# Performance work log

Hardware: AMD Instinct MI355X
Metric: run time of the kernel (lower is better)

The kernel has to match this reference:

```python
import jax, jax.numpy as jnp
import numpy as np

B, H, W, C = 4, 64, 64, 256
C8 = C // 8

def setup_inputs() -> dict:
    key = jax.random.key(0)
    k1, k2, k3, k4 = jax.random.split(key, 4)
    # glorot-uniform-ish init for 1x1 conv kernels stored as [Cin, Cout]
    def glorot(k, cin, cout):
        lim = np.sqrt(6.0 / (cin + cout)).astype(np.float32)
        return jax.random.uniform(k, (cin, cout), jnp.float32, -lim, lim)
    return {
        "x": jax.random.normal(k1, (B, H, W, C), jnp.float32),
        "kernel_f": glorot(k2, C, C8),
        "kernel_g": glorot(k3, C, C8),
        "kernel_h": glorot(k4, C, C),
        "gamma": jnp.zeros((1,), jnp.float32),
    }

def reference(x, kernel_f, kernel_g, kernel_h, gamma):
    b, h, w, c = x.shape
    n = h * w
    xf = x.reshape(b, n, c)                       # [B, N, C]
    # 1x1 convs == per-position matmuls
    f = jnp.einsum('bnc,cd->bnd', xf, kernel_f)   # [B, N, C/8]
    g = jnp.einsum('bnc,cd->bnd', xf, kernel_g)   # [B, N, C/8]
    hh = jnp.einsum('bnc,cd->bnd', xf, kernel_h)  # [B, N, C]
    s = jnp.einsum('bnd,bmd->bnm', g, f)          # [B, N, N]
    beta = jax.nn.softmax(s, axis=-1)
    o = jnp.einsum('bnm,bmc->bnc', beta, hh)      # [B, N, C]
    o = o.reshape(b, h, w, c)
    return gamma * o + x
```

## Files before the change

### kernel.cpp

```cpp
#include <hip/hip_runtime.h>
#include <hip/hip_bf16.h>

typedef __bf16 bf16x8 __attribute__((ext_vector_type(8)));
typedef float f32x4 __attribute__((ext_vector_type(4)));
typedef float f32x16 __attribute__((ext_vector_type(16)));
typedef unsigned short u16;
typedef unsigned int u32;

__device__ __forceinline__ u16 f2bf_rne(float f){
  union { float f; u32 u; } v; v.f = f;
  u32 r = v.u + 0x7fffu + ((v.u >> 16) & 1u);
  return (u16)(r >> 16);
}
__device__ __forceinline__ u32 pack2(float a, float b){
  return __builtin_amdgcn_perm(__float_as_uint(a), __float_as_uint(b), 0x03020706u);
}
#define BARRIER_LGKM() asm volatile("s_waitcnt lgkmcnt(0)\n\ts_barrier" ::: "memory")

__global__ __launch_bounds__(512) void prep_kernel(
    const float* __restrict__ Wf, const float* __restrict__ Wg,
    const float* __restrict__ Wh, u16* __restrict__ Wfrag){
  const int cc = blockIdx.x;
  const int t = threadIdx.x;
  const int kk = t >> 6, lane = t & 63;
  const int L = lane & 15, quad = lane >> 4;
  const int n = cc * 16 + L;
  u32 pk[4];
  #pragma unroll
  for (int j2 = 0; j2 < 4; ++j2){
    float v[2];
    #pragma unroll
    for (int h = 0; h < 2; ++h){
      int k = kk * 32 + quad * 8 + j2 * 2 + h;
      if (n < 256)      v[h] = Wh[k * 256 + n];
      else if (n < 288) v[h] = Wf[k * 32 + (n - 256)];
      else              v[h] = Wg[k * 32 + (n - 288)];
    }
    pk[j2] = (u32)f2bf_rne(v[0]) | ((u32)f2bf_rne(v[1]) << 16);
  }
  uint4* dst = (uint4*)(Wfrag + ((size_t)(cc * 8 + kk) * 64 + lane) * 8);
  *dst = make_uint4(pk[0], pk[1], pk[2], pk[3]);
}

__global__ __launch_bounds__(512) void proj_kernel(
    const float* __restrict__ x, const u16* __restrict__ Wfrag,
    u16* __restrict__ Qg, u16* __restrict__ Kg, u16* __restrict__ Vfrag)
{
  __shared__ __align__(16) u16 smem[256 * 72];
  u16 (*xb)[264] = (u16(*)[264])smem;
  u16 (*Vr)[72]  = (u16(*)[72])smem;

  const int tid = threadIdx.x;
  const int lane = tid & 63, wave = tid >> 6;
  const int L = lane & 15, quad = lane >> 4;
  const int rowgrp = wave >> 1, colhalf = wave & 1;
  const int n0 = blockIdx.x * 64;

  const float4* xsrc = (const float4*)(x + (size_t)n0 * 256);
  #pragma unroll
  for (int j = 0; j < 8; ++j){
    int idx = j * 512 + tid;
    int row = idx >> 6, col4 = idx & 63;
    float4 v = xsrc[idx];
    u32 p0 = (u32)f2bf_rne(v.x) | ((u32)f2bf_rne(v.y) << 16);
    u32 p1 = (u32)f2bf_rne(v.z) | ((u32)f2bf_rne(v.w) << 16);
    *(uint2*)&xb[row][col4 * 4] = make_uint2(p0, p1);
  }
  __syncthreads();

  f32x4 acc[10];
  #pragma unroll
  for (int cc = 0; cc < 10; ++cc) acc[cc] = (f32x4){0.f, 0.f, 0.f, 0.f};

  #pragma unroll
  for (int kk = 0; kk < 8; ++kk){
    bf16x8 a = *(const bf16x8*)&xb[rowgrp * 16 + L][kk * 32 + quad * 8];
    #pragma unroll
    for (int cc = 0; cc < 10; ++cc){
      int ccg = colhalf * 10 + cc;
      bf16x8 bfr = *(const bf16x8*)(Wfrag + ((size_t)(ccg * 8 + kk) * 64 + lane) * 8);
      acc[cc] = __builtin_amdgcn_mfma_f32_16x16x32_bf16(a, bfr, acc[cc], 0, 0, 0);
    }
  }

  if (colhalf){
    #pragma unroll
    for (int cc = 6; cc < 10; ++cc){
      int ccg = 10 + cc;
      u16* dst = (ccg < 18) ? Kg : Qg;
      float sc = (ccg < 18) ? 1.0f : 1.44269504088896f;
      int c = (ccg & 1) * 16 + L;
      #pragma unroll
      for (int r = 0; r < 4; ++r){
        int row = n0 + rowgrp * 16 + quad * 4 + r;
        dst[(size_t)row * 32 + c] = f2bf_rne(acc[cc][r] * sc);
      }
    }
  }

  __syncthreads();

  {
    const int cmax = colhalf ? 6 : 10;
    for (int cc = 0; cc < cmax; ++cc){
      int ccg = colhalf * 10 + cc;
      int c = ccg * 16 + L;
      #pragma unroll
      for (int r = 0; r < 4; ++r){
        int tn = rowgrp * 16 + quad * 4 + r;
        int p  = ((tn & 15) << 2) | (tn >> 4);
        Vr[c][p] = f2bf_rne(acc[cc][r]);
      }
    }
  }
  __syncthreads();

  u16* Vblk = Vfrag + (size_t)blockIdx.x * (256 * 64);
  #pragma unroll
  for (int i = 0; i < 4; ++i){
    int idx = i * 512 + tid;
    *(uint4*)(Vblk + (size_t)idx * 8) = *(const uint4*)&Vr[idx & 255][(idx >> 8) * 8];
  }
}

__global__ __launch_bounds__(512) void flash_kernel(
    const u16* __restrict__ Qg, const u16* __restrict__ Kg, const u16* __restrict__ Vfrag,
    const float* __restrict__ x, const float* __restrict__ gamma, float* __restrict__ out)
{
  constexpr float SH = -92.33248261689366f;
  __shared__ __align__(16) char smem[65536];
  u16 (*Plds)[2][64][72] = (u16 (*)[2][64][72])smem;
  float (*Osh)[256] = (float (*)[256])smem;
  __shared__ float Lsh[2][64];

  const int tid = threadIdx.x, lane = tid & 63, wave = tid >> 6;
  const int L = lane & 15, quad = lane >> 4;
  const int m32 = lane & 31, h32 = lane >> 5;
  const int half = wave >> 2, wv = wave & 3;

  const int id = blockIdx.x;
  const int xcd = id & 7;
  const int b = xcd >> 1;
  const int qt = (xcd & 1) * 32 + (id >> 3);
  const int q0 = qt * 64;

  const u16* Qb = Qg + (size_t)(b * 4096) * 32;
  const u16* Kb = Kg + (size_t)(b * 4096) * 32;
  const u16* Vb = Vfrag + (size_t)b * (64 * 256 * 64);
  const float gm = gamma[0];

  const int g0 = half * 32;

  bf16x8 qa = *(const bf16x8*)(Qb + (size_t)(q0 + wv * 16 + L) * 32 + quad * 8);
  const u16* kp0 = Kb + (size_t)(g0 * 64 + L) * 32 + quad * 8;
  bf16x8 kc0 = *(const bf16x8*)(kp0);
  bf16x8 kc1 = *(const bf16x8*)(kp0 + 512);
  bf16x8 kc2 = *(const bf16x8*)(kp0 + 1024);
  bf16x8 kc3 = *(const bf16x8*)(kp0 + 1536);

  bf16x8 vfc[8];
  {
    const u16* Vt = Vb + (size_t)g0 * (256 * 64);
    #pragma unroll
    for (int ks = 0; ks < 4; ++ks){
      const u16* vrow = Vt + (size_t)((ks * 2 + h32) * 256 + wv * 64 + m32) * 8;
      vfc[ks * 2]     = *(const bf16x8*)(vrow);
      vfc[ks * 2 + 1] = *(const bf16x8*)(vrow + 32 * 8);
    }
  }

  f32x16 acc[4];
  #pragma unroll
  for (int t = 0; t < 4; ++t)
    #pragma unroll
    for (int i = 0; i < 16; ++i) acc[t][i] = 0.f;
  float lsum[4] = {0.f, 0.f, 0.f, 0.f};
  const f32x4 zero = (f32x4){0.f, 0.f, 0.f, 0.f};

  for (int kt = 0; kt < 32; ++kt){
    const int g = g0 + kt;
    u16 (*Pw)[72] = Plds[half][kt & 1];

    f32x4 s0 = __builtin_amdgcn_mfma_f32_16x16x32_bf16(qa, kc0, zero, 0, 0, 0);
    f32x4 s1 = __builtin_amdgcn_mfma_f32_16x16x32_bf16(qa, kc1, zero, 0, 0, 0);
    f32x4 s2 = __builtin_amdgcn_mfma_f32_16x16x32_bf16(qa, kc2, zero, 0, 0, 0);
    f32x4 s3 = __builtin_amdgcn_mfma_f32_16x16x32_bf16(qa, kc3, zero, 0, 0, 0);

    if (kt < 31){
      const u16* kpn = Kb + (size_t)((g + 1) * 64 + L) * 32 + quad * 8;
      kc0 = *(const bf16x8*)(kpn);
      kc1 = *(const bf16x8*)(kpn + 512);
      kc2 = *(const bf16x8*)(kpn + 1024);
      kc3 = *(const bf16x8*)(kpn + 1536);
    }

    #pragma unroll
    for (int r = 0; r < 4; ++r){
      float p0 = __builtin_amdgcn_exp2f(s0[r] + SH);
      float p1 = __builtin_amdgcn_exp2f(s1[r] + SH);
      float p2 = __builtin_amdgcn_exp2f(s2[r] + SH);
      float p3 = __builtin_amdgcn_exp2f(s3[r] + SH);
      lsum[r] += (p0 + p1) + (p2 + p3);
      *(uint2*)&Pw[wv * 16 + quad * 4 + r][L * 4] =
          make_uint2(pack2(p0, p1), pack2(p2, p3));
    }

    BARRIER_LGKM();

    #pragma unroll
    for (int ks = 0; ks < 4; ++ks){
      bf16x8 af0 = *(const bf16x8*)&Pw[m32][ks * 16 + h32 * 8];
      bf16x8 af1 = *(const bf16x8*)&Pw[32 + m32][ks * 16 + h32 * 8];
      acc[0] = __builtin_amdgcn_mfma_f32_32x32x16_bf16(af0, vfc[ks*2],   acc[0], 0, 0, 0);
      acc[1] = __builtin_amdgcn_mfma_f32_32x32x16_bf16(af0, vfc[ks*2+1], acc[1], 0, 0, 0);
      acc[2] = __builtin_amdgcn_mfma_f32_32x32x16_bf16(af1, vfc[ks*2],   acc[2], 0, 0, 0);
      acc[3] = __builtin_amdgcn_mfma_f32_32x32x16_bf16(af1, vfc[ks*2+1], acc[3], 0, 0, 0);
    }

    if (kt < 31){
      const u16* Vn = Vb + (size_t)(g + 1) * (256 * 64);
      #pragma unroll
      for (int ks = 0; ks < 4; ++ks){
        const u16* vrow = Vn + (size_t)((ks * 2 + h32) * 256 + wv * 64 + m32) * 8;
        vfc[ks * 2]     = *(const bf16x8*)(vrow);
        vfc[ks * 2 + 1] = *(const bf16x8*)(vrow + 32 * 8);
      }
    }
  }

  BARRIER_LGKM();

  #pragma unroll
  for (int r = 0; r < 4; ++r){
    lsum[r] += __shfl_xor(lsum[r], 1);
    lsum[r] += __shfl_xor(lsum[r], 2);
    lsum[r] += __shfl_xor(lsum[r], 4);
    lsum[r] += __shfl_xor(lsum[r], 8);
  }
  if (L == 0){
    #pragma unroll
    for (int r = 0; r < 4; ++r) Lsh[half][wv * 16 + quad * 4 + r] = lsum[r];
  }
  if (half == 1){
    #pragma unroll
    for (int t = 0; t < 4; ++t){
      const int qi = t >> 1, ci = t & 1;
      #pragma unroll
      for (int rg = 0; rg < 16; ++rg){
        int row = qi * 32 + (rg & 3) + 8 * (rg >> 2) + 4 * h32;
        Osh[row][wv * 64 + ci * 32 + m32] = acc[t][rg];
      }
    }
  }
  __syncthreads();
  if (wave == 0){
    float li = gm / (Lsh[0][lane] + Lsh[1][lane]);
    Lsh[0][lane] = li;
  }
  __syncthreads();
  if (half == 0){
    #pragma unroll
    for (int t = 0; t < 4; ++t){
      const int qi = t >> 1, ci = t & 1;
      #pragma unroll
      for (int rg = 0; rg < 16; ++rg){
        int row = qi * 32 + (rg & 3) + 8 * (rg >> 2) + 4 * h32;
        int col = wv * 64 + ci * 32 + m32;
        Osh[row][col] = (acc[t][rg] + Osh[row][col]) * Lsh[0][row];
      }
    }
  }
  __syncthreads();
  const size_t base = ((size_t)(b * 4096) + q0) * 256;
  const float4* xs = (const float4*)(x + base);
  float4* od = (float4*)(out + base);
  const float4* Of = (const float4*)&Osh[0][0];
  #pragma unroll
  for (int i = 0; i < 8; ++i){
    int idx = i * 512 + tid;
    float4 o = Of[idx], xv = xs[idx];
    o.x += xv.x; o.y += xv.y; o.z += xv.z; o.w += xv.w;
    od[idx] = o;
  }
}

extern "C" void kernel_launch(void* const* d_in, const int* in_sizes, int n_in,
                              void* d_out, int out_size, void* d_ws, size_t ws_size,
                              hipStream_t stream) {
  const float* x     = (const float*)d_in[0];
  const float* Wf    = (const float*)d_in[1];
  const float* Wg    = (const float*)d_in[2];
  const float* Wh    = (const float*)d_in[3];
  const float* gamma = (const float*)d_in[4];
  float* out = (float*)d_out;

  u16* p = (u16*)d_ws;
  u16* Qg    = p;  p += 16384 * 32;
  u16* Kg    = p;  p += 16384 * 32;
  u16* Vfrag = p;  p += 4 * 64 * 256 * 64;
  u16* Wfrag = p;  p += 20 * 8 * 64 * 8;

  prep_kernel<<<20, 512, 0, stream>>>(Wf, Wg, Wh, Wfrag);
  proj_kernel<<<256, 512, 0, stream>>>(x, Wfrag, Qg, Kg, Vfrag);
  flash_kernel<<<256, 512, 0, stream>>>(Qg, Kg, Vfrag, x, gamma, out);
}
```

Baseline: 151.3 us.

## Split flash attention KV range across four wave groups with 1024-thread blocks

New measurement: 233.0 us. 53.9% more time.

```diff
diff --git a/kernel.cpp b/kernel.cpp
--- a/kernel.cpp
+++ b/kernel.cpp
@@ -123,20 +123,20 @@
   }
 }
 
-__global__ __launch_bounds__(512) void flash_kernel(
+__global__ __launch_bounds__(1024) void flash_kernel(
     const u16* __restrict__ Qg, const u16* __restrict__ Kg, const u16* __restrict__ Vfrag,
     const float* __restrict__ x, const float* __restrict__ gamma, float* __restrict__ out)
 {
   constexpr float SH = -92.33248261689366f;
-  __shared__ __align__(16) char smem[65536];
+  __shared__ __align__(16) char smem[73728];
   u16 (*Plds)[2][64][72] = (u16 (*)[2][64][72])smem;
   float (*Osh)[256] = (float (*)[256])smem;
-  __shared__ float Lsh[2][64];
+  __shared__ float Lsh[4][64];
 
   const int tid = threadIdx.x, lane = tid & 63, wave = tid >> 6;
   const int L = lane & 15, quad = lane >> 4;
   const int m32 = lane & 31, h32 = lane >> 5;
-  const int half = wave >> 2, wv = wave & 3;
+  const int quarter = wave >> 2, wv = wave & 3;
 
   const int id = blockIdx.x;
   const int xcd = id & 7;
@@ -149,7 +149,7 @@
   const u16* Vb = Vfrag + (size_t)b * (64 * 256 * 64);
   const float gm = gamma[0];
 
-  const int g0 = half * 32;
+  const int g0 = quarter * 16;
 
   bf16x8 qa = *(const bf16x8*)(Qb + (size_t)(q0 + wv * 16 + L) * 32 + quad * 8);
   const u16* kp0 = Kb + (size_t)(g0 * 64 + L) * 32 + quad * 8;
@@ -177,16 +177,16 @@
   float lsum[4] = {0.f, 0.f, 0.f, 0.f};
   const f32x4 zero = (f32x4){0.f, 0.f, 0.f, 0.f};
 
-  for (int kt = 0; kt < 32; ++kt){
+  for (int kt = 0; kt < 16; ++kt){
     const int g = g0 + kt;
-    u16 (*Pw)[72] = Plds[half][kt & 1];
+    u16 (*Pw)[72] = Plds[quarter][kt & 1];
 
     f32x4 s0 = __builtin_amdgcn_mfma_f32_16x16x32_bf16(qa, kc0, zero, 0, 0, 0);
     f32x4 s1 = __builtin_amdgcn_mfma_f32_16x16x32_bf16(qa, kc1, zero, 0, 0, 0);
     f32x4 s2 = __builtin_amdgcn_mfma_f32_16x16x32_bf16(qa, kc2, zero, 0, 0, 0);
     f32x4 s3 = __builtin_amdgcn_mfma_f32_16x16x32_bf16(qa, kc3, zero, 0, 0, 0);
 
-    if (kt < 31){
+    if (kt < 15){
       const u16* kpn = Kb + (size_t)((g + 1) * 64 + L) * 32 + quad * 8;
       kc0 = *(const bf16x8*)(kpn);
       kc1 = *(const bf16x8*)(kpn + 512);
@@ -217,7 +217,7 @@
       acc[3] = __builtin_amdgcn_mfma_f32_32x32x16_bf16(af1, vfc[ks*2+1], acc[3], 0, 0, 0);
     }
 
-    if (kt < 31){
+    if (kt < 15){
       const u16* Vn = Vb + (size_t)(g + 1) * (256 * 64);
       #pragma unroll
       for (int ks = 0; ks < 4; ++ks){
@@ -227,8 +227,6 @@
       }
     }
   }
-
-  BARRIER_LGKM();
 
   #pragma unroll
   for (int r = 0; r < 4; ++r){
@@ -239,9 +237,12 @@
   }
   if (L == 0){
     #pragma unroll
-    for (int r = 0; r < 4; ++r) Lsh[half][wv * 16 + quad * 4 + r] = lsum[r];
-  }
-  if (half == 1){
+    for (int r = 0; r < 4; ++r) Lsh[quarter][wv * 16 + quad * 4 + r] = lsum[r];
+  }
+
+  BARRIER_LGKM();
+
+  if (quarter == 3){
     #pragma unroll
     for (int t = 0; t < 4; ++t){
       const int qi = t >> 1, ci = t & 1;
@@ -252,13 +253,36 @@
       }
     }
   }
-  __syncthreads();
-  if (wave == 0){
-    float li = gm / (Lsh[0][lane] + Lsh[1][lane]);
-    Lsh[0][lane] = li;
-  }
-  __syncthreads();
-  if (half == 0){
+  float li_w0 = 0.f;
+  if (wave == 0)
+    li_w0 = gm / (Lsh[0][lane] + Lsh[1][lane] + Lsh[2][lane] + Lsh[3][lane]);
+  __syncthreads();
+  if (wave == 0) Lsh[0][lane] = li_w0;
+  if (quarter == 2){
+    #pragma unroll
+    for (int t = 0; t < 4; ++t){
+      const int qi = t >> 1, ci = t & 1;
+      #pragma unroll
+      for (int rg = 0; rg < 16; ++rg){
+        int row = qi * 32 + (rg & 3) + 8 * (rg >> 2) + 4 * h32;
+        Osh[row][wv * 64 + ci * 32 + m32] += acc[t][rg];
+      }
+    }
+  }
+  __syncthreads();
+  if (quarter == 1){
+    #pragma unroll
+    for (int t = 0; t < 4; ++t){
+      const int qi = t >> 1, ci = t & 1;
+      #pragma unroll
+      for (int rg = 0; rg < 16; ++rg){
+        int row = qi * 32 + (rg & 3) + 8 * (rg >> 2) + 4 * h32;
+        Osh[row][wv * 64 + ci * 32 + m32] += acc[t][rg];
+      }
+    }
+  }
+  __syncthreads();
+  if (quarter == 0){
     #pragma unroll
     for (int t = 0; t < 4; ++t){
       const int qi = t >> 1, ci = t & 1;
@@ -276,8 +300,8 @@
   float4* od = (float4*)(out + base);
   const float4* Of = (const float4*)&Osh[0][0];
   #pragma unroll
-  for (int i = 0; i < 8; ++i){
-    int idx = i * 512 + tid;
+  for (int i = 0; i < 4; ++i){
+    int idx = i * 1024 + tid;
     float4 o = Of[idx], xv = xs[idx];
     o.x += xv.x; o.y += xv.y; o.z += xv.z; o.w += xv.w;
     od[idx] = o;
@@ -302,5 +326,5 @@
 
   prep_kernel<<<20, 512, 0, stream>>>(Wf, Wg, Wh, Wfrag);
   proj_kernel<<<256, 512, 0, stream>>>(x, Wfrag, Qg, Kg, Vfrag);
-  flash_kernel<<<256, 512, 0, stream>>>(Qg, Kg, Vfrag, x, gamma, out);
-}
+  flash_kernel<<<256, 1024, 0, stream>>>(Qg, Kg, Vfrag, x, gamma, out);
+}
```

## Split flash kernel over channel halves and stage V tiles through LDS

Applied to the files above, without the earlier changes.

After: 182.9 us. +20.9%, slower.

```diff
diff --git a/kernel.cpp b/kernel.cpp
--- a/kernel.cpp
+++ b/kernel.cpp
@@ -15,7 +15,10 @@
 __device__ __forceinline__ u32 pack2(float a, float b){
   return __builtin_amdgcn_perm(__float_as_uint(a), __float_as_uint(b), 0x03020706u);
 }
-#define BARRIER_LGKM() asm volatile("s_waitcnt lgkmcnt(0)\n\ts_barrier" ::: "memory")
+__device__ __forceinline__ void load_lds16(const void* g, void* l){
+  __builtin_amdgcn_global_load_lds((const __attribute__((address_space(1))) void*)g,
+                                   (__attribute__((address_space(3))) void*)l, 16, 0, 0);
+}
 
 __global__ __launch_bounds__(512) void prep_kernel(
     const float* __restrict__ Wf, const float* __restrict__ Wg,
@@ -128,71 +131,66 @@
     const float* __restrict__ x, const float* __restrict__ gamma, float* __restrict__ out)
 {
   constexpr float SH = -92.33248261689366f;
-  __shared__ __align__(16) char smem[65536];
-  u16 (*Plds)[2][64][72] = (u16 (*)[2][64][72])smem;
-  float (*Osh)[256] = (float (*)[256])smem;
+  __shared__ __align__(16) u16 Vlds[2][8192];
+  __shared__ __align__(16) u16 Plds[2][2][64][72];
   __shared__ float Lsh[2][64];
 
   const int tid = threadIdx.x, lane = tid & 63, wave = tid >> 6;
   const int L = lane & 15, quad = lane >> 4;
   const int m32 = lane & 31, h32 = lane >> 5;
-  const int half = wave >> 2, wv = wave & 3;
+  const int qg = wave >> 2, wv = wave & 3;
 
   const int id = blockIdx.x;
   const int xcd = id & 7;
   const int b = xcd >> 1;
-  const int qt = (xcd & 1) * 32 + (id >> 3);
-  const int q0 = qt * 64;
+  const int ch = (id >> 3) & 1;
+  const int qt = (xcd & 1) * 16 + (id >> 4);
+  const int q0 = qt * 128;
 
   const u16* Qb = Qg + (size_t)(b * 4096) * 32;
   const u16* Kb = Kg + (size_t)(b * 4096) * 32;
   const u16* Vb = Vfrag + (size_t)b * (64 * 256 * 64);
   const float gm = gamma[0];
 
-  const int g0 = half * 32;
-
-  bf16x8 qa = *(const bf16x8*)(Qb + (size_t)(q0 + wv * 16 + L) * 32 + quad * 8);
-  const u16* kp0 = Kb + (size_t)(g0 * 64 + L) * 32 + quad * 8;
+  bf16x8 qa = *(const bf16x8*)(Qb + (size_t)(q0 + qg * 64 + wv * 16 + L) * 32 + quad * 8);
+
+  {
+    const u16* src = Vb + wave * 2048 + ch * 1024 + lane * 8;
+    load_lds16(src,       &Vlds[0][wave * 1024]);
+    load_lds16(src + 512, &Vlds[0][wave * 1024 + 512]);
+    asm volatile("" ::: "memory");
+  }
+  const u16* kp0 = Kb + (size_t)(0 * 64 + L) * 32 + quad * 8;
   bf16x8 kc0 = *(const bf16x8*)(kp0);
   bf16x8 kc1 = *(const bf16x8*)(kp0 + 512);
   bf16x8 kc2 = *(const bf16x8*)(kp0 + 1024);
   bf16x8 kc3 = *(const bf16x8*)(kp0 + 1536);
 
-  bf16x8 vfc[8];
-  {
-    const u16* Vt = Vb + (size_t)g0 * (256 * 64);
-    #pragma unroll
-    for (int ks = 0; ks < 4; ++ks){
-      const u16* vrow = Vt + (size_t)((ks * 2 + h32) * 256 + wv * 64 + m32) * 8;
-      vfc[ks * 2]     = *(const bf16x8*)(vrow);
-      vfc[ks * 2 + 1] = *(const bf16x8*)(vrow + 32 * 8);
-    }
-  }
-
-  f32x16 acc[4];
-  #pragma unroll
-  for (int t = 0; t < 4; ++t)
+  f32x16 acc[2];
+  #pragma unroll
+  for (int t = 0; t < 2; ++t)
     #pragma unroll
     for (int i = 0; i < 16; ++i) acc[t][i] = 0.f;
   float lsum[4] = {0.f, 0.f, 0.f, 0.f};
   const f32x4 zero = (f32x4){0.f, 0.f, 0.f, 0.f};
 
-  for (int kt = 0; kt < 32; ++kt){
-    const int g = g0 + kt;
-    u16 (*Pw)[72] = Plds[half][kt & 1];
+  int buf = 0;
+  for (int kt = 0; kt < 63; ++kt){
+    u16 (*Pw)[72] = Plds[qg][kt & 1];
 
     f32x4 s0 = __builtin_amdgcn_mfma_f32_16x16x32_bf16(qa, kc0, zero, 0, 0, 0);
     f32x4 s1 = __builtin_amdgcn_mfma_f32_16x16x32_bf16(qa, kc1, zero, 0, 0, 0);
     f32x4 s2 = __builtin_amdgcn_mfma_f32_16x16x32_bf16(qa, kc2, zero, 0, 0, 0);
     f32x4 s3 = __builtin_amdgcn_mfma_f32_16x16x32_bf16(qa, kc3, zero, 0, 0, 0);
 
-    if (kt < 31){
-      const u16* kpn = Kb + (size_t)((g + 1) * 64 + L) * 32 + quad * 8;
+    {
+      const u16* kpn = Kb + (size_t)((kt + 1) * 64 + L) * 32 + quad * 8;
       kc0 = *(const bf16x8*)(kpn);
       kc1 = *(const bf16x8*)(kpn + 512);
       kc2 = *(const bf16x8*)(kpn + 1024);
       kc3 = *(const bf16x8*)(kpn + 1536);
     }
+    asm volatile("" ::: "memory");
 
     #pragma unroll
     for (int r = 0; r < 4; ++r){
@@ -205,30 +203,54 @@
           make_uint2(pack2(p0, p1), pack2(p2, p3));
     }
 
-    BARRIER_LGKM();
-
+    asm volatile("s_waitcnt vmcnt(4) lgkmcnt(0)\n\ts_barrier" ::: "memory");
+
+    {
+      const u16* Vn = Vb + (size_t)(kt + 1) * 16384 + wave * 2048 + ch * 1024 + lane * 8;
+      load_lds16(Vn,       &Vlds[buf ^ 1][wave * 1024]);
+      load_lds16(Vn + 512, &Vlds[buf ^ 1][wave * 1024 + 512]);
+      asm volatile("" ::: "memory");
+    }
+
+    const u16* Vls = &Vlds[buf][0];
     #pragma unroll
     for (int ks = 0; ks < 4; ++ks){
+      bf16x8 vf  = *(const bf16x8*)(Vls + ((ks * 2 + h32) * 128 + wv * 32 + m32) * 8);
       bf16x8 af0 = *(const bf16x8*)&Pw[m32][ks * 16 + h32 * 8];
       bf16x8 af1 = *(const bf16x8*)&Pw[32 + m32][ks * 16 + h32 * 8];
-      acc[0] = __builtin_amdgcn_mfma_f32_32x32x16_bf16(af0, vfc[ks*2],   acc[0], 0, 0, 0);
-      acc[1] = __builtin_amdgcn_mfma_f32_32x32x16_bf16(af0, vfc[ks*2+1], acc[1], 0, 0, 0);
-      acc[2] = __builtin_amdgcn_mfma_f32_32x32x16_bf16(af1, vfc[ks*2],   acc[2], 0, 0, 0);
-      acc[3] = __builtin_amdgcn_mfma_f32_32x32x16_bf16(af1, vfc[ks*2+1], acc[3], 0, 0, 0);
-    }
-
-    if (kt < 31){
-      const u16* Vn = Vb + (size_t)(g + 1) * (256 * 64);
-      #pragma unroll
-      for (int ks = 0; ks < 4; ++ks){
-        const u16* vrow = Vn + (size_t)((ks * 2 + h32) * 256 + wv * 64 + m32) * 8;
-        vfc[ks * 2]     = *(const bf16x8*)(vrow);
-        vfc[ks * 2 + 1] = *(const bf16x8*)(vrow + 32 * 8);
-      }
-    }
-  }
-
-  BARRIER_LGKM();
+      acc[0] = __builtin_amdgcn_mfma_f32_32x32x16_bf16(af0, vf, acc[0], 0, 0, 0);
+      acc[1] = __builtin_amdgcn_mfma_f32_32x32x16_bf16(af1, vf, acc[1], 0, 0, 0);
+    }
+    buf ^= 1;
+  }
+
+  {
+    u16 (*Pw)[72] = Plds[qg][63 & 1];
+    f32x4 s0 = __builtin_amdgcn_mfma_f32_16x16x32_bf16(qa, kc0, zero, 0, 0, 0);
+    f32x4 s1 = __builtin_amdgcn_mfma_f32_16x16x32_bf16(qa, kc1, zero, 0, 0, 0);
+    f32x4 s2 = __builtin_amdgcn_mfma_f32_16x16x32_bf16(qa, kc2, zero, 0, 0, 0);
+    f32x4 s3 = __builtin_amdgcn_mfma_f32_16x16x32_bf16(qa, kc3, zero, 0, 0, 0);
+    #pragma unroll
+    for (int r = 0; r < 4; ++r){
+      float p0 = __builtin_amdgcn_exp2f(s0[r] + SH);
+      float p1 = __builtin_amdgcn_exp2f(s1[r] + SH);
+      float p2 = __builtin_amdgcn_exp2f(s2[r] + SH);
+      float p3 = __builtin_amdgcn_exp2f(s3[r] + SH);
+      lsum[r] += (p0 + p1) + (p2 + p3);
+      *(uint2*)&Pw[wv * 16 + quad * 4 + r][L * 4] =
+          make_uint2(pack2(p0, p1), pack2(p2, p3));
+    }
+    asm volatile("s_waitcnt vmcnt(0) lgkmcnt(0)\n\ts_barrier" ::: "memory");
+    const u16* Vls = &Vlds[buf][0];
+    #pragma unroll
+    for (int ks = 0; ks < 4; ++ks){
+      bf16x8 vf  = *(const bf16x8*)(Vls + ((ks * 2 + h32) * 128 + wv * 32 + m32) * 8);
+      bf16x8 af0 = *(const bf16x8*)&Pw[m32][ks * 16 + h32 * 8];
+      bf16x8 af1 = *(const bf16x8*)&Pw[32 + m32][ks * 16 + h32 * 8];
+      acc[0] = __builtin_amdgcn_mfma_f32_32x32x16_bf16(af0, vf, acc[0], 0, 0, 0);
+      acc[1] = __builtin_amdgcn_mfma_f32_32x32x16_bf16(af1, vf, acc[1], 0, 0, 0);
+    }
+  }
 
   #pragma unroll
   for (int r = 0; r < 4; ++r){
@@ -239,48 +261,22 @@
   }
   if (L == 0){
     #pragma unroll
-    for (int r = 0; r < 4; ++r) Lsh[half][wv * 16 + quad * 4 + r] = lsum[r];
-  }
-  if (half == 1){
-    #pragma unroll
-    for (int t = 0; t < 4; ++t){
-      const int qi = t >> 1, ci = t & 1;
-      #pragma unroll
-      for (int rg = 0; rg < 16; ++rg){
-        int row = qi * 32 + (rg & 3) + 8 * (rg >> 2) + 4 * h32;
-        Osh[row][wv * 64 + ci * 32 + m32] = acc[t][rg];
-      }
-    }
+    for (int r = 0; r < 4; ++r) Lsh[qg][wv * 16 + quad * 4 + r] = lsum[r];
   }
   __syncthreads();
-  if (wave == 0){
-    float li = gm / (Lsh[0][lane] + Lsh[1][lane]);
-    Lsh[0][lane] = li;
-  }
-  __syncthreads();
-  if (half == 0){
-    #pragma unroll
-    for (int t = 0; t < 4; ++t){
-      const int qi = t >> 1, ci = t & 1;
-      #pragma unroll
-      for (int rg = 0; rg < 16; ++rg){
-        int row = qi * 32 + (rg & 3) + 8 * (rg >> 2) + 4 * h32;
-        int col = wv * 64 + ci * 32 + m32;
-        Osh[row][col] = (acc[t][rg] + Osh[row][col]) * Lsh[0][row];
-      }
-    }
-  }
-  __syncthreads();
-  const size_t base = ((size_t)(b * 4096) + q0) * 256;
-  const float4* xs = (const float4*)(x + base);
-  float4* od = (float4*)(out + base);
-  const float4* Of = (const float4*)&Osh[0][0];
-  #pragma unroll
-  for (int i = 0; i < 8; ++i){
-    int idx = i * 512 + tid;
-    float4 o = Of[idx], xv = xs[idx];
-    o.x += xv.x; o.y += xv.y; o.z += xv.z; o.w += xv.w;
-    od[idx] = o;
+
+  const size_t base = (((size_t)(b * 4096) + q0)) * 256 + ch * 128;
+  const int col = wv * 32 + m32;
+  #pragma unroll
+  for (int t = 0; t < 2; ++t){
+    #pragma unroll
+    for (int rg = 0; rg < 16; ++rg){
+      int rloc = t * 32 + (rg & 3) + 8 * (rg >> 2) + 4 * h32;
+      int row = qg * 64 + rloc;
+      float li = gm / Lsh[qg][rloc];
+      size_t off = base + (size_t)row * 256 + col;
+      out[off] = acc[t][rg] * li + x[off];
+    }
   }
 }
 
```
